# Performance work log

Measured on AMD Instinct MI355X. Metric: run time of the kernel, lower is better.

The kernel has to match this reference:

```python
import jax, jax.numpy as jnp
import numpy as np

EPS = 1e-12  # torch F.normalize default eps


def l2_normalize_c(x):
    # F.normalize over channel dim (dim=1): x / max(||x||_2, eps)
    nrm = jnp.sqrt(jnp.sum(x * x, axis=1, keepdims=True))
    return x / jnp.maximum(nrm, EPS)


def resize_bilinear_ac(x, H, W):
    # bilinear, align_corners=True (matches torch F.interpolate)
    n, c, h, w = x.shape
    ys = jnp.linspace(0.0, h - 1.0, H)
    xs = jnp.linspace(0.0, w - 1.0, W)
    y0 = jnp.floor(ys).astype(jnp.int32)
    y1 = jnp.minimum(y0 + 1, h - 1)
    wy = (ys - y0.astype(ys.dtype))[:, None]          # [H,1]
    x0 = jnp.floor(xs).astype(jnp.int32)
    x1 = jnp.minimum(x0 + 1, w - 1)
    wx = xs - x0.astype(xs.dtype)                      # [W]
    rows = x[:, :, y0, :] * (1.0 - wy) + x[:, :, y1, :] * wy   # [n,c,H,w]
    return rows[:, :, :, x0] * (1.0 - wx) + rows[:, :, :, x1] * wx  # [n,c,H,W]


def unfold_3x3_d2(x):
    # nn.Unfold(kernel=3, dilation=2, padding=2, stride=1) viewed as [n,c,9,h,w]
    n, c, h, w = x.shape
    xp = jnp.pad(x, ((0, 0), (0, 0), (2, 2), (2, 2)))
    return jnp.stack(
        [xp[:, :, dy:dy + h, dx:dx + w] for dy in (0, 2, 4) for dx in (0, 2, 4)],
        axis=2,
    )  # [n,c,9,h,w], kernel index row-major (ky*3+kx) matching torch unfold


def setup_inputs() -> dict:
    key = jax.random.key(0)
    k1, k2, k3, k4, k5 = jax.random.split(key, 5)
    return {
        "c1": jax.random.normal(k1, (4, 256, 128, 128), dtype=jnp.float32),
        "c2": jax.random.normal(k2, (4, 512, 64, 64), dtype=jnp.float32),
        "out": jax.random.normal(k3, (4, 256, 64, 64), dtype=jnp.float32),
        "w_refine": jax.random.normal(k4, (32, 256), dtype=jnp.float32) * 0.05,
        "w_refine2": jax.random.normal(k5, (32, 512), dtype=jnp.float32) * 0.05,
    }


def reference(c1, c2, out, w_refine, w_refine2):
    n, _, h, w = c1.shape
    # 1x1 conv (no bias) + L2 normalize over channels
    q = l2_normalize_c(jnp.einsum("nchw,kc->nkhw", c1, w_refine))       # [n,32,h,w]
    c2u = resize_bilinear_ac(c2, h, w)
    kft = l2_normalize_c(jnp.einsum("nchw,kc->nkhw", c2u, w_refine2))    # [n,32,h,w]
    kpat = unfold_3x3_d2(kft)                                            # [n,32,9,h,w]
    energy = jnp.einsum("nchw,nckhw->nkhw", q, kpat)                     # [n,9,h,w]
    att = jax.nn.softmax(energy, axis=1)
    outu = resize_bilinear_ac(out, h, w)                                 # [n,C,h,w]
    vpat = unfold_3x3_d2(outu)                                           # [n,C,9,h,w]
    return jnp.einsum("nkhw,nckhw->nchw", att, vpat)
```

## Files before the change

### kernel.cpp

```cpp
#include <hip/hip_runtime.h>
#include <hip/hip_bf16.h>


typedef float f32x4 __attribute__((ext_vector_type(4)));
typedef float f32x2 __attribute__((ext_vector_type(2)));

#define SCL (63.0f / 127.0f)

__global__ __launch_bounds__(512) void k_q(const float* __restrict__ c1,
                                           const float* __restrict__ wr,
                                           float* __restrict__ q) {
    __shared__ float red[4 * 32 * 130];
    int b = blockIdx.x;
    int n = b >> 7;
    int pblk = (b & 127) * 128;
    int t = threadIdx.x;
    int lane = t & 63;
    int w = t >> 6;
    int cg = __builtin_amdgcn_readfirstlane(w & 3);
    int og = __builtin_amdgcn_readfirstlane(w >> 2);

    const float* src = c1 + ((size_t)n * 256 + cg * 64) * 16384 + pblk + lane * 2;
    const float* wp  = wr + (og * 16) * 256 + cg * 64;

    float acc0[16], acc1[16];
#pragma unroll
    for (int o = 0; o < 16; ++o) { acc0[o] = 0.f; acc1[o] = 0.f; }
#pragma unroll 4
    for (int c = 0; c < 64; ++c) {
        f32x2 v = *(const f32x2*)(src + (size_t)c * 16384);
#pragma unroll
        for (int o = 0; o < 16; ++o) {
            float wv = wp[o * 256 + c];
            acc0[o] = fmaf(v[0], wv, acc0[o]);
            acc1[o] = fmaf(v[1], wv, acc1[o]);
        }
    }
#pragma unroll
    for (int o = 0; o < 16; ++o) {
        f32x2 pr = { acc0[o], acc1[o] };
        *(f32x2*)&red[(cg * 32 + og * 16 + o) * 130 + lane * 2] = pr;
    }
    __syncthreads();

    if (t < 256) {
        int px = t & 127, half = t >> 7;
        float v[16];
#pragma unroll
        for (int o = 0; o < 16; ++o) {
            v[o] = red[(0 * 32 + half * 16 + o) * 130 + px]
                 + red[(1 * 32 + half * 16 + o) * 130 + px]
                 + red[(2 * 32 + half * 16 + o) * 130 + px]
                 + red[(3 * 32 + half * 16 + o) * 130 + px];
        }
        float* dst = q + ((size_t)n * 16384 + pblk + px) * 32 + half * 16;
#pragma unroll
        for (int j = 0; j < 4; ++j) {
            f32x4 o4 = { v[4*j], v[4*j+1], v[4*j+2], v[4*j+3] };
            *(f32x4*)(dst + 4 * j) = o4;
        }
    }
}

__global__ __launch_bounds__(1024) void k_kfs(const float* __restrict__ c2,
                                              const float* __restrict__ wr2,
                                              float* __restrict__ kfs) {
    __shared__ float red[8 * 32 * 66];
    int b = blockIdx.x;
    int n = b >> 6;
    int pblk = (b & 63) * 64;
    int t = threadIdx.x;
    int lane = t & 63;
    int w = t >> 6;
    int cg = __builtin_amdgcn_readfirstlane(w & 7);
    int og = __builtin_amdgcn_readfirstlane(w >> 3);

    const float* src = c2 + ((size_t)n * 512 + cg * 64) * 4096 + pblk + lane;
    const float* wp  = wr2 + (og * 16) * 512 + cg * 64;

    float acc[16];
#pragma unroll
    for (int o = 0; o < 16; ++o) acc[o] = 0.f;
#pragma unroll 4
    for (int c = 0; c < 64; ++c) {
        float v = src[(size_t)c * 4096];
#pragma unroll
        for (int o = 0; o < 16; ++o)
            acc[o] = fmaf(v, wp[o * 512 + c], acc[o]);
    }
#pragma unroll
    for (int o = 0; o < 16; ++o)
        red[(cg * 32 + og * 16 + o) * 66 + lane] = acc[o];
    __syncthreads();

    if (t < 512) {
        int px = t & 63, seg = t >> 6;
        float v[4];
#pragma unroll
        for (int j = 0; j < 4; ++j) {
            float r = 0.f;
#pragma unroll
            for (int g = 0; g < 8; ++g) r += red[(g * 32 + seg * 4 + j) * 66 + px];
            v[j] = r;
        }
        f32x4 o4 = { v[0], v[1], v[2], v[3] };
        *(f32x4*)(kfs + ((size_t)n * 4096 + pblk + px) * 32 + seg * 4) = o4;
    }
}

__global__ __launch_bounds__(256) void k_upnorm(const float* __restrict__ kfs,
                                                float* __restrict__ kft) {
    int p   = blockIdx.x * 256 + threadIdx.x;
    int n   = p >> 14;
    int rem = p & 16383;
    int y = rem >> 7, x = rem & 127;
    float syf = SCL * (float)y; int y0 = (int)syf; float fy = syf - (float)y0;
    int y1 = min(y0 + 1, 63);
    float sxf = SCL * (float)x; int x0 = (int)sxf; float fx = sxf - (float)x0;
    int x1 = min(x0 + 1, 63);
    size_t base = (size_t)n * 4096 * 32;
    const f32x4* p00 = (const f32x4*)(kfs + base + ((size_t)(y0 * 64 + x0)) * 32);
    const f32x4* p01 = (const f32x4*)(kfs + base + ((size_t)(y0 * 64 + x1)) * 32);
    const f32x4* p10 = (const f32x4*)(kfs + base + ((size_t)(y1 * 64 + x0)) * 32);
    const f32x4* p11 = (const f32x4*)(kfs + base + ((size_t)(y1 * 64 + x1)) * 32);
    float w00 = (1.f-fy)*(1.f-fx), w01 = (1.f-fy)*fx, w10 = fy*(1.f-fx), w11 = fy*fx;
    float v[32]; float s = 0.f;
#pragma unroll
    for (int j = 0; j < 8; ++j) {
        f32x4 a = p00[j], b = p01[j], c = p10[j], d = p11[j];
#pragma unroll
        for (int tt = 0; tt < 4; ++tt) {
            float r = a[tt]*w00 + b[tt]*w01 + c[tt]*w10 + d[tt]*w11;
            v[4*j + tt] = r;
            s = fmaf(r, r, s);
        }
    }
    float inv = 1.0f / fmaxf(sqrtf(s), 1e-12f);
    f32x4* dst = (f32x4*)(kft + (size_t)p * 32);
#pragma unroll
    for (int j = 0; j < 8; ++j) {
        f32x4 t = { v[4*j]*inv, v[4*j+1]*inv, v[4*j+2]*inv, v[4*j+3]*inv };
        dst[j] = t;
    }
}

__global__ __launch_bounds__(256) void k_att_w(const float* __restrict__ q,
                                               const float* __restrict__ kft,
                                               float* __restrict__ wbuf) {
    __shared__ float wsc[256 * 17];
    int t = threadIdx.x;
    int p = blockIdx.x * 256 + t;
    int n = p >> 14, rem = p & 16383;
    int y = rem >> 7, x = rem & 127;

    int ybase = min((int)(SCL * (float)max(y - 2, 0)), 60);
    int xbase = min((int)(SCL * (float)max(x - 2, 0)), 60);

    float qv[32];
    const f32x4* qp = (const f32x4*)(q + (size_t)p * 32);
    float qs = 0.f;
#pragma unroll
    for (int j = 0; j < 8; ++j) {
        f32x4 v = qp[j];
        qv[4*j] = v[0]; qv[4*j+1] = v[1]; qv[4*j+2] = v[2]; qv[4*j+3] = v[3];
        qs = fmaf(v[0], v[0], qs); qs = fmaf(v[1], v[1], qs);
        qs = fmaf(v[2], v[2], qs); qs = fmaf(v[3], v[3], qs);
    }
    float qinv = 1.0f / fmaxf(sqrtf(qs), 1e-12f);
#pragma unroll
    for (int j = 0; j < 32; ++j) qv[j] *= qinv;

    float e[9];
#pragma unroll
    for (int k = 0; k < 9; ++k) {
        int ky = k / 3, kx = k % 3;
        int ny = y + 2 * ky - 2, nx = x + 2 * kx - 2;
        float acc = 0.f;
        if (ny >= 0 && ny < 128 && nx >= 0 && nx < 128) {
            const f32x4* kp = (const f32x4*)(kft + ((size_t)n * 16384 + ny * 128 + nx) * 32);
#pragma unroll
            for (int j = 0; j < 8; ++j) {
                f32x4 v = kp[j];
                acc = fmaf(v[0], qv[4*j],   acc);
                acc = fmaf(v[1], qv[4*j+1], acc);
                acc = fmaf(v[2], qv[4*j+2], acc);
                acc = fmaf(v[3], qv[4*j+3], acc);
            }
        }
        e[k] = acc;
    }
    float m = e[0];
#pragma unroll
    for (int k = 1; k < 9; ++k) m = fmaxf(m, e[k]);
    float ssum = 0.f;
#pragma unroll
    for (int k = 0; k < 9; ++k) { e[k] = __expf(e[k] - m); ssum += e[k]; }
    float rinv = 1.0f / ssum;

    float* wp = wsc + t * 17;
#pragma unroll
    for (int i = 0; i < 16; ++i) wp[i] = 0.f;
#pragma unroll
    for (int ky = 0; ky < 3; ++ky) {
        int ny = y + 2 * ky - 2;
        if (ny < 0 || ny > 127) continue;
        float syf = SCL * (float)ny; int iy0 = (int)syf; float fy = syf - (float)iy0;
        int iy1 = min(iy0 + 1, 63);
        int r0 = (iy0 - ybase) * 4, r1 = (iy1 - ybase) * 4;
#pragma unroll
        for (int kx = 0; kx < 3; ++kx) {
            int nx = x + 2 * kx - 2;
            if (nx < 0 || nx > 127) continue;
            float sxf = SCL * (float)nx; int ix0 = (int)sxf; float fx = sxf - (float)ix0;
            int ix1 = min(ix0 + 1, 63);
            float a = e[ky * 3 + kx] * rinv;
            wp[r0 + (ix0 - xbase)] += a * (1.f - fy) * (1.f - fx);
            wp[r0 + (ix1 - xbase)] += a * (1.f - fy) * fx;
            wp[r1 + (ix0 - xbase)] += a * fy * (1.f - fx);
            wp[r1 + (ix1 - xbase)] += a * fy * fx;
        }
    }
#pragma unroll
    for (int i = 0; i < 16; ++i) wbuf[i * 65536 + p] = wp[i];
}

__global__ __launch_bounds__(256) void k_agg(const float* __restrict__ wbuf,
                                             const float* __restrict__ outp,
                                             float* __restrict__ res) {
    __shared__ float wlds[128 * 17];
    __shared__ float tile[8 * 260];
    int b = blockIdx.x;
    int cg = b & 3, y = (b >> 2) & 127, n = b >> 9;
    int t = threadIdx.x;
    int x = t & 127, half = t >> 7;

    int ybase = min((int)(SCL * (float)max(y - 2, 0)), 60);
    int pix = n * 16384 + y * 128;

#pragma unroll
    for (int k = 0; k < 8; ++k) {
        int u = t + 256 * k;
        int i = u >> 7, xx = u & 127;
        wlds[xx * 17 + i] = wbuf[i * 65536 + pix + xx];
    }
    __syncthreads();
    float w16[16];
#pragma unroll
    for (int i = 0; i < 16; ++i) w16[i] = wlds[x * 17 + i];
    int xb = min((int)(SCL * (float)max(x - 2, 0)), 60);

    const float* ob = outp + ((size_t)n * 256 + cg * 64) * 4096 + ybase * 64;
    float* rb = res + ((size_t)n * 256 + cg * 64) * 16384 + y * 128 + x;

#pragma unroll 1
    for (int batch = 0; batch < 8; ++batch) {
        __syncthreads();
        const float* src = ob + (size_t)batch * 8 * 4096;
#pragma unroll
        for (int k = 0; k < 2; ++k) {
            int u = t + 256 * k;
            int cl = u >> 6, seg = u & 63;
            f32x4 v = *(const f32x4*)(src + (size_t)cl * 4096 + seg * 4);
            *(f32x4*)&tile[cl * 260 + seg * 4] = v;
        }
        __syncthreads();
#pragma unroll
        for (int cl = 0; cl < 4; ++cl) {
            int c = half * 4 + cl;
            const float* tp = tile + c * 260 + xb;
            float acc = 0.f;
#pragma unroll
            for (int r = 0; r < 4; ++r) {
                acc = fmaf(tp[r*64 + 0], w16[r*4 + 0], acc);
                acc = fmaf(tp[r*64 + 1], w16[r*4 + 1], acc);
                acc = fmaf(tp[r*64 + 2], w16[r*4 + 2], acc);
                acc = fmaf(tp[r*64 + 3], w16[r*4 + 3], acc);
            }
            rb[(size_t)(batch * 8 + c) * 16384] = acc;
        }
    }
}

extern "C" void kernel_launch(void* const* d_in, const int* in_sizes, int n_in,
                              void* d_out, int out_size, void* d_ws, size_t ws_size,
                              hipStream_t stream) {
    const float* c1   = (const float*)d_in[0];
    const float* c2   = (const float*)d_in[1];
    const float* outp = (const float*)d_in[2];
    const float* wr   = (const float*)d_in[3];
    const float* wr2  = (const float*)d_in[4];
    float* res = (float*)d_out;

    float* q_ws   = (float*)d_ws;
    float* kfs_ws = (float*)((char*)d_ws + 8388608);
    float* kft_ws = (float*)((char*)d_ws + 8388608 + 2097152);
    float* w_ws   = (float*)((char*)d_ws + 8388608 + 2097152 + 8388608);

    hipLaunchKernelGGL(k_q,      dim3(512),  dim3(512),  0, stream, c1, wr, q_ws);
    hipLaunchKernelGGL(k_kfs,    dim3(256),  dim3(1024), 0, stream, c2, wr2, kfs_ws);
    hipLaunchKernelGGL(k_upnorm, dim3(256),  dim3(256),  0, stream, kfs_ws, kft_ws);
    hipLaunchKernelGGL(k_att_w,  dim3(256),  dim3(256),  0, stream, q_ws, kft_ws, w_ws);
    hipLaunchKernelGGL(k_agg,    dim3(2048), dim3(256),  0, stream, w_ws, outp, res);
}
```

Measured before the change: 87.16 us.

## Split each pixel across four threads in upsample-normalize and attention-weight kernels

New measurement: 81.21 us. 6.8% less time.

```diff
diff --git a/kernel.cpp b/kernel.cpp
--- a/kernel.cpp
+++ b/kernel.cpp
@@ -110,23 +110,24 @@
 
 __global__ __launch_bounds__(256) void k_upnorm(const float* __restrict__ kfs,
                                                 float* __restrict__ kft) {
-    int p   = blockIdx.x * 256 + threadIdx.x;
-    int n   = p >> 14;
+    int g = blockIdx.x * 256 + threadIdx.x;
+    int p = g >> 2, qt = g & 3;
+    int n = p >> 14;
     int rem = p & 16383;
     int y = rem >> 7, x = rem & 127;
     float syf = SCL * (float)y; int y0 = (int)syf; float fy = syf - (float)y0;
     int y1 = min(y0 + 1, 63);
     float sxf = SCL * (float)x; int x0 = (int)sxf; float fx = sxf - (float)x0;
     int x1 = min(x0 + 1, 63);
-    size_t base = (size_t)n * 4096 * 32;
+    size_t base = (size_t)n * 4096 * 32 + qt * 8;
     const f32x4* p00 = (const f32x4*)(kfs + base + ((size_t)(y0 * 64 + x0)) * 32);
     const f32x4* p01 = (const f32x4*)(kfs + base + ((size_t)(y0 * 64 + x1)) * 32);
     const f32x4* p10 = (const f32x4*)(kfs + base + ((size_t)(y1 * 64 + x0)) * 32);
     const f32x4* p11 = (const f32x4*)(kfs + base + ((size_t)(y1 * 64 + x1)) * 32);
     float w00 = (1.f-fy)*(1.f-fx), w01 = (1.f-fy)*fx, w10 = fy*(1.f-fx), w11 = fy*fx;
-    float v[32]; float s = 0.f;
-#pragma unroll
-    for (int j = 0; j < 8; ++j) {
+    float v[8]; float s = 0.f;
+#pragma unroll
+    for (int j = 0; j < 2; ++j) {
         f32x4 a = p00[j], b = p01[j], c = p10[j], d = p11[j];
 #pragma unroll
         for (int tt = 0; tt < 4; ++tt) {
@@ -135,10 +136,12 @@
             s = fmaf(r, r, s);
         }
     }
+    s += __shfl_xor(s, 1, 4);
+    s += __shfl_xor(s, 2, 4);
     float inv = 1.0f / fmaxf(sqrtf(s), 1e-12f);
-    f32x4* dst = (f32x4*)(kft + (size_t)p * 32);
-#pragma unroll
-    for (int j = 0; j < 8; ++j) {
+    f32x4* dst = (f32x4*)(kft + (size_t)p * 32 + qt * 8);
+#pragma unroll
+    for (int j = 0; j < 2; ++j) {
         f32x4 t = { v[4*j]*inv, v[4*j+1]*inv, v[4*j+2]*inv, v[4*j+3]*inv };
         dst[j] = t;
     }
@@ -147,57 +150,57 @@
 __global__ __launch_bounds__(256) void k_att_w(const float* __restrict__ q,
                                                const float* __restrict__ kft,
                                                float* __restrict__ wbuf) {
-    __shared__ float wsc[256 * 17];
+    __shared__ float wsc[64 * 17];
     int t = threadIdx.x;
-    int p = blockIdx.x * 256 + t;
+    int g = blockIdx.x * 256 + t;
+    int p = g >> 2, qt = g & 3;
     int n = p >> 14, rem = p & 16383;
     int y = rem >> 7, x = rem & 127;
+    int pixL = t >> 2;
 
     int ybase = min((int)(SCL * (float)max(y - 2, 0)), 60);
     int xbase = min((int)(SCL * (float)max(x - 2, 0)), 60);
 
-    float qv[32];
-    const f32x4* qp = (const f32x4*)(q + (size_t)p * 32);
+    const f32x4* qp = (const f32x4*)(q + (size_t)p * 32 + qt * 8);
+    f32x4 q0 = qp[0], q1 = qp[1];
     float qs = 0.f;
 #pragma unroll
-    for (int j = 0; j < 8; ++j) {
-        f32x4 v = qp[j];
-        qv[4*j] = v[0]; qv[4*j+1] = v[1]; qv[4*j+2] = v[2]; qv[4*j+3] = v[3];
-        qs = fmaf(v[0], v[0], qs); qs = fmaf(v[1], v[1], qs);
-        qs = fmaf(v[2], v[2], qs); qs = fmaf(v[3], v[3], qs);
-    }
-    float qinv = 1.0f / fmaxf(sqrtf(qs), 1e-12f);
-#pragma unroll
-    for (int j = 0; j < 32; ++j) qv[j] *= qinv;
-
-    float e[9];
+    for (int tt = 0; tt < 4; ++tt) { qs = fmaf(q0[tt], q0[tt], qs); qs = fmaf(q1[tt], q1[tt], qs); }
+
+    float d[9];
 #pragma unroll
     for (int k = 0; k < 9; ++k) {
         int ky = k / 3, kx = k % 3;
         int ny = y + 2 * ky - 2, nx = x + 2 * kx - 2;
         float acc = 0.f;
         if (ny >= 0 && ny < 128 && nx >= 0 && nx < 128) {
-            const f32x4* kp = (const f32x4*)(kft + ((size_t)n * 16384 + ny * 128 + nx) * 32);
-#pragma unroll
-            for (int j = 0; j < 8; ++j) {
-                f32x4 v = kp[j];
-                acc = fmaf(v[0], qv[4*j],   acc);
-                acc = fmaf(v[1], qv[4*j+1], acc);
-                acc = fmaf(v[2], qv[4*j+2], acc);
-                acc = fmaf(v[3], qv[4*j+3], acc);
-            }
-        }
-        e[k] = acc;
-    }
-    float m = e[0];
-#pragma unroll
-    for (int k = 1; k < 9; ++k) m = fmaxf(m, e[k]);
+            const f32x4* kp = (const f32x4*)(kft + ((size_t)n * 16384 + ny * 128 + nx) * 32 + qt * 8);
+            f32x4 a = kp[0], b = kp[1];
+            acc = fmaf(a[0], q0[0], acc); acc = fmaf(a[1], q0[1], acc);
+            acc = fmaf(a[2], q0[2], acc); acc = fmaf(a[3], q0[3], acc);
+            acc = fmaf(b[0], q1[0], acc); acc = fmaf(b[1], q1[1], acc);
+            acc = fmaf(b[2], q1[2], acc); acc = fmaf(b[3], q1[3], acc);
+        }
+        d[k] = acc;
+    }
+    qs += __shfl_xor(qs, 1, 4); qs += __shfl_xor(qs, 2, 4);
+#pragma unroll
+    for (int k = 0; k < 9; ++k) {
+        d[k] += __shfl_xor(d[k], 1, 4);
+        d[k] += __shfl_xor(d[k], 2, 4);
+    }
+    float qinv = 1.0f / fmaxf(sqrtf(qs), 1e-12f);
+
+    float e[9];
+    float m = d[0] * qinv;
+#pragma unroll
+    for (int k = 0; k < 9; ++k) { e[k] = d[k] * qinv; if (k) m = fmaxf(m, e[k]); }
     float ssum = 0.f;
 #pragma unroll
     for (int k = 0; k < 9; ++k) { e[k] = __expf(e[k] - m); ssum += e[k]; }
     float rinv = 1.0f / ssum;
 
-    float* wp = wsc + t * 17;
+    float* wp = wsc + pixL * 17;
 #pragma unroll
     for (int i = 0; i < 16; ++i) wp[i] = 0.f;
 #pragma unroll
@@ -220,8 +223,15 @@
             wp[r1 + (ix1 - xbase)] += a * fy * fx;
         }
     }
-#pragma unroll
-    for (int i = 0; i < 16; ++i) wbuf[i * 65536 + p] = wp[i];
+    __syncthreads();
+
+    int px = t & 63, i0 = t >> 6;
+    int pb = blockIdx.x * 64;
+#pragma unroll
+    for (int r = 0; r < 4; ++r) {
+        int i = r * 4 + i0;
+        wbuf[i * 65536 + pb + px] = wsc[px * 17 + i];
+    }
 }
 
 __global__ __launch_bounds__(256) void k_agg(const float* __restrict__ wbuf,
@@ -298,7 +308,7 @@
 
     hipLaunchKernelGGL(k_q,      dim3(512),  dim3(512),  0, stream, c1, wr, q_ws);
     hipLaunchKernelGGL(k_kfs,    dim3(256),  dim3(1024), 0, stream, c2, wr2, kfs_ws);
-    hipLaunchKernelGGL(k_upnorm, dim3(256),  dim3(256),  0, stream, kfs_ws, kft_ws);
-    hipLaunchKernelGGL(k_att_w,  dim3(256),  dim3(256),  0, stream, q_ws, kft_ws, w_ws);
+    hipLaunchKernelGGL(k_upnorm, dim3(1024), dim3(256),  0, stream, kfs_ws, kft_ws);
+    hipLaunchKernelGGL(k_att_w,  dim3(1024), dim3(256),  0, stream, q_ws, kft_ws, w_ws);
     hipLaunchKernelGGL(k_agg,    dim3(2048), dim3(256),  0, stream, w_ws, outp, res);
 }
```
